# Optimization experiments

Measured on AMD Instinct MI355X. Metric: run time of the kernel, lower is better.

Reference implementation:

```python
import jax, jax.numpy as jnp
import numpy as np

N = 100000      # nodes
E = 1600000     # edges (avg degree 16)
IN_FEATS = 128
HEADS = 4
OUT_FEATS = 16
NEG_SLOPE = 0.2
EPS = 1e-16


def setup_inputs() -> dict:
    key = jax.random.key(0)
    k1, k2, k3, k4, k5, k6 = jax.random.split(key, 6)
    feat = jax.random.normal(k1, (N, IN_FEATS), dtype=jnp.float32)
    # xavier-ish scale for params
    W = jax.random.normal(k2, (IN_FEATS, HEADS * OUT_FEATS), dtype=jnp.float32) * 0.1
    attn_l = jax.random.normal(k3, (1, HEADS, OUT_FEATS), dtype=jnp.float32) * 0.1
    attn_r = jax.random.normal(k4, (1, HEADS, OUT_FEATS), dtype=jnp.float32) * 0.1
    src_index = jax.random.randint(k5, (E,), 0, N, dtype=jnp.int32)
    trg_index = jax.random.randint(k6, (E,), 0, N, dtype=jnp.int32)
    return {"feat": feat, "W": W, "attn_l": attn_l, "attn_r": attn_r,
            "src_index": src_index, "trg_index": trg_index}


def reference(feat, W, attn_l, attn_r, src_index, trg_index):
    # dropout layers are identity in eval mode
    n = feat.shape[0]
    h = (feat @ W).reshape(n, HEADS, OUT_FEATS)            # [N,H,F]
    el = jnp.sum(h * attn_l, axis=-1)                      # [N,H]
    er = jnp.sum(h * attn_r, axis=-1)                      # [N,H]
    s = el[src_index] + er[trg_index]                      # [E,H] edge scores
    s = jnp.where(s > 0, s, NEG_SLOPE * s)                 # LeakyReLU(0.2)
    # neighborhood-aware softmax over incoming edges of each target node
    s = s - jnp.max(s)                                     # global max shift (as in source)
    e = jnp.exp(s)                                         # [E,H]
    denom = jax.ops.segment_sum(e, trg_index, num_segments=n)  # [N,H]
    attn = e / (denom[trg_index] + EPS)                    # [E,H]
    # weighted aggregation of lifted source features into target nodes
    msg = h[src_index] * attn[:, :, None]                  # [E,H,F]
    h_prime = jax.ops.segment_sum(msg, trg_index, num_segments=n)  # [N,H,F]
    return h_prime.reshape(n, HEADS * OUT_FEATS)
```

## Files before the change

kernel.cpp:

```cpp
#include <hip/hip_runtime.h>

typedef unsigned short ushort_t;
typedef __attribute__((ext_vector_type(8))) short bf16x8;
typedef __attribute__((ext_vector_type(4))) float f32x4v;

static __device__ __forceinline__ float bf2f(ushort_t u) {
  union { unsigned int i; float f; } v; v.i = ((unsigned int)u) << 16; return v.f;
}
static __device__ __forceinline__ ushort_t f2bf(float f) {
  union { float f; unsigned int i; } v; v.f = f;
  unsigned int r = v.i + 0x7FFFu + ((v.i >> 16) & 1u);
  return (ushort_t)(r >> 16);
}
static __device__ __forceinline__ float leaky(float s) {
  return s > 0.f ? s : 0.2f * s;
}

__global__ __launch_bounds__(256) void packw_hist(
    const float* __restrict__ W, const float* __restrict__ attnl,
    const float* __restrict__ attnr, ushort_t* __restrict__ wfrag,
    const int* __restrict__ trg, int E, int nbkt,
    int* __restrict__ blockHist, int nb3, int epb)
{
  const int b = blockIdx.x;
  const int t = threadIdx.x;
  if (b == nb3) {
    const int kc = t >> 6, l = t & 63;
    const int q = l >> 4, n = l & 15;
    #pragma unroll
    for (int tile = 0; tile < 5; ++tile) {
      #pragma unroll
      for (int j = 0; j < 8; ++j) {
        const int k = kc * 32 + q * 8 + j;
        float v = 0.f;
        if (tile < 4) {
          v = W[k * 64 + tile * 16 + n];
        } else if (n < 4) {
          for (int f = 0; f < 16; ++f)
            v += W[k * 64 + n * 16 + f] * attnl[n * 16 + f];
        } else if (n < 8) {
          const int hd = n - 4;
          for (int f = 0; f < 16; ++f)
            v += W[k * 64 + hd * 16 + f] * attnr[hd * 16 + f];
        }
        wfrag[((tile * 4 + kc) * 64 + l) * 8 + j] = f2bf(v);
      }
    }
    return;
  }
  __shared__ int hist[256];
  hist[t] = 0;
  __syncthreads();
  const int start = b * epb;
  const int end = min(start + epb, E);
  for (int e = start + t; e < end; e += 256)
    atomicAdd(&hist[trg[e] >> 9], 1);
  __syncthreads();
  if (t < nbkt) blockHist[b * nbkt + t] = hist[t];
}

__global__ __launch_bounds__(64) void bucket_scan(
    int* __restrict__ blockHist, int nb3, int nbkt, int* __restrict__ colTotal)
{
  const int b = blockIdx.x;
  const int l = threadIdx.x;
  int carry = 0;
  for (int r = 0; r * 64 < nb3; ++r) {
    const int i = r * 64 + l;
    int v = (i < nb3) ? blockHist[i * nbkt + b] : 0;
    int incl = v;
    #pragma unroll
    for (int d = 1; d < 64; d <<= 1) {
      int u = __shfl_up(incl, d, 64);
      if (l >= d) incl += u;
    }
    if (i < nb3) blockHist[i * nbkt + b] = carry + incl - v;
    carry += __shfl(incl, 63, 64);
  }
  if (l == 0) colTotal[b] = carry;
}

__global__ __launch_bounds__(64) void bucket_base(
    const int* __restrict__ colTotal, int nbkt, int* __restrict__ bucketBase,
    int* __restrict__ rowoff, int N, int E)
{
  const int l = threadIdx.x;
  int carry = 0;
  for (int r = 0; r * 64 < nbkt; ++r) {
    const int i = r * 64 + l;
    int v = (i < nbkt) ? colTotal[i] : 0;
    int incl = v;
    #pragma unroll
    for (int d = 1; d < 64; d <<= 1) {
      int u = __shfl_up(incl, d, 64);
      if (l >= d) incl += u;
    }
    if (i < nbkt) bucketBase[i] = carry + incl - v;
    carry += __shfl(incl, 63, 64);
  }
  if (l == 0) { bucketBase[nbkt] = carry; rowoff[N] = E; }
}

__global__ __launch_bounds__(256) void bucket_scatter(
    const int* __restrict__ src, const int* __restrict__ trg, int E, int nbkt,
    const int* __restrict__ blockHist, const int* __restrict__ bucketBase,
    unsigned int* __restrict__ binned, int epb)
{
  __shared__ int cursor[256];
  const int t = threadIdx.x, b = blockIdx.x;
  if (t < nbkt) cursor[t] = bucketBase[t] + blockHist[b * nbkt + t];
  __syncthreads();
  const int start = b * epb;
  const int end = min(start + epb, E);
  for (int e = start + t; e < end; e += 256) {
    const int ti = trg[e];
    const int bkt = ti >> 9;
    const int pos = atomicAdd(&cursor[bkt], 1);
    binned[pos] = ((unsigned int)src[e] << 9) | (unsigned int)(ti & 511);
  }
}

__global__ __launch_bounds__(256) void gat_linear(
    const float* __restrict__ feat, const ushort_t* __restrict__ wfrag,
    ushort_t* __restrict__ h_out, float* __restrict__ el, float* __restrict__ er,
    float* __restrict__ blockmax2, int N)
{
  __shared__ ushort_t sFb[64 * 136];
  __shared__ float wmax[8];
  const int t = threadIdx.x;
  const int b = blockIdx.x;
  const int w = t >> 6, l = t & 63;
  const int q = l >> 4, m = l & 15;

  const float4* gF = (const float4*)(feat + (size_t)b * 64 * 128);
  #pragma unroll
  for (int i = 0; i < 8; ++i) {
    const int idx = i * 256 + t;
    const int node = idx >> 5, off = idx & 31;
    float4 v = make_float4(0.f, 0.f, 0.f, 0.f);
    if (b * 64 + node < N) v = gF[idx];
    unsigned int p0 = ((unsigned int)f2bf(v.y) << 16) | f2bf(v.x);
    unsigned int p1 = ((unsigned int)f2bf(v.w) << 16) | f2bf(v.z);
    *(uint2*)(sFb + node * 136 + off * 4) = make_uint2(p0, p1);
  }
  __syncthreads();

  bf16x8 a[4];
  const ushort_t* arow = sFb + (w * 16 + m) * 136 + q * 8;
  #pragma unroll
  for (int kc = 0; kc < 4; ++kc)
    a[kc] = *(const bf16x8*)(arow + kc * 32);

  #pragma unroll
  for (int tile = 0; tile < 4; ++tile) {
    f32x4v acc = {0.f, 0.f, 0.f, 0.f};
    #pragma unroll
    for (int kc = 0; kc < 4; ++kc) {
      bf16x8 bfr = *(const bf16x8*)(wfrag + ((tile * 4 + kc) * 64 + l) * 8);
      acc = __builtin_amdgcn_mfma_f32_16x16x32_bf16(a[kc], bfr, acc, 0, 0, 0);
    }
    #pragma unroll
    for (int r = 0; r < 4; ++r) {
      const int gn = b * 64 + w * 16 + q * 4 + r;
      if (gn < N) h_out[(size_t)gn * 64 + tile * 16 + m] = f2bf(acc[r]);
    }
  }

  f32x4v acc4 = {0.f, 0.f, 0.f, 0.f};
  #pragma unroll
  for (int kc = 0; kc < 4; ++kc) {
    bf16x8 bfr = *(const bf16x8*)(wfrag + ((4 * 4 + kc) * 64 + l) * 8);
    acc4 = __builtin_amdgcn_mfma_f32_16x16x32_bf16(a[kc], bfr, acc4, 0, 0, 0);
  }
  float mel = -1e30f, mer = -1e30f;
  #pragma unroll
  for (int r = 0; r < 4; ++r) {
    const int gn = b * 64 + w * 16 + q * 4 + r;
    const float v = acc4[r];
    if (m < 4) {
      if (gn < N) el[gn * 4 + m] = v;
      mel = fmaxf(mel, v);
    } else if (m < 8) {
      if (gn < N) er[gn * 4 + (m - 4)] = v;
      mer = fmaxf(mer, v);
    }
  }
  #pragma unroll
  for (int o = 1; o <= 32; o <<= 1) {
    mel = fmaxf(mel, __shfl_xor(mel, o, 64));
    mer = fmaxf(mer, __shfl_xor(mer, o, 64));
  }
  if (l == 0) { wmax[w * 2] = mel; wmax[w * 2 + 1] = mer; }
  __syncthreads();
  if (t == 0) {
    float aa = fmaxf(fmaxf(wmax[0], wmax[2]), fmaxf(wmax[4], wmax[6]));
    float cc = fmaxf(fmaxf(wmax[1], wmax[3]), fmaxf(wmax[5], wmax[7]));
    blockmax2[b * 2] = aa;
    blockmax2[b * 2 + 1] = cc;
  }
}

__global__ __launch_bounds__(512) void fine_scatter(
    const unsigned int* __restrict__ binned, const int* __restrict__ bucketBase,
    int* __restrict__ rowoff, int* __restrict__ csrsrc, int N,
    const float* __restrict__ blockmax2, int nbL, float* __restrict__ gmaxM)
{
  __shared__ int cnt[512];
  __shared__ int ws[8];
  __shared__ float wmg[16];
  const int t = threadIdx.x, b = blockIdx.x;
  const int l = t & 63, w = t >> 6;
  const int base = bucketBase[b];
  const int end = bucketBase[b + 1];
  cnt[t] = 0;
  if (b == 0) {
    float mel = -1e30f, mer = -1e30f;
    for (int i = t; i < nbL; i += 512) {
      mel = fmaxf(mel, blockmax2[i * 2]);
      mer = fmaxf(mer, blockmax2[i * 2 + 1]);
    }
    #pragma unroll
    for (int o = 1; o <= 32; o <<= 1) {
      mel = fmaxf(mel, __shfl_xor(mel, o, 64));
      mer = fmaxf(mer, __shfl_xor(mer, o, 64));
    }
    if (l == 0) { wmg[w * 2] = mel; wmg[w * 2 + 1] = mer; }
  }
  __syncthreads();
  if (b == 0 && t == 0) {
    float aa = -1e30f, cc = -1e30f;
    for (int i = 0; i < 8; ++i) {
      aa = fmaxf(aa, wmg[i * 2]);
      cc = fmaxf(cc, wmg[i * 2 + 1]);
    }
    gmaxM[0] = fmaxf(0.f, aa + cc);
  }
  for (int i = base + t; i < end; i += 512)
    atomicAdd(&cnt[binned[i] & 511u], 1);
  __syncthreads();
  const int v = cnt[t];
  int incl = v;
  #pragma unroll
  for (int d = 1; d < 64; d <<= 1) {
    int u = __shfl_up(incl, d, 64);
    if (l >= d) incl += u;
  }
  if (l == 63) ws[w] = incl;
  __syncthreads();
  int woff = 0;
  for (int i = 0; i < w; ++i) woff += ws[i];
  const int loc = woff + incl - v;
  cnt[t] = loc;
  const int gt = b * 512 + t;
  if (gt < N) rowoff[gt] = base + loc;
  __syncthreads();
  for (int i = base + t; i < end; i += 512) {
    const unsigned int pv = binned[i];
    const int lt = (int)(pv & 511u);
    const int pos = base + atomicAdd(&cnt[lt], 1);
    csrsrc[pos] = (int)(pv >> 9);
  }
}

#define FMA8(hv, p) do { \
  union { unsigned int i; float f; } c_; \
  c_.i = (hv).x << 16;          a0 += c_.f * (p); \
  c_.i = (hv).x & 0xffff0000u;  a1 += c_.f * (p); \
  c_.i = (hv).y << 16;          a2 += c_.f * (p); \
  c_.i = (hv).y & 0xffff0000u;  a3 += c_.f * (p); \
  c_.i = (hv).z << 16;          a4 += c_.f * (p); \
  c_.i = (hv).z & 0xffff0000u;  a5 += c_.f * (p); \
  c_.i = (hv).w << 16;          a6 += c_.f * (p); \
  c_.i = (hv).w & 0xffff0000u;  a7 += c_.f * (p); \
} while (0)

__global__ __launch_bounds__(256) void gat_agg(
    const int* __restrict__ csrsrc, const int* __restrict__ rowoff,
    const float4* __restrict__ el4, const float4* __restrict__ er4,
    const ushort_t* __restrict__ hbf, const float* __restrict__ gmaxM,
    float* __restrict__ out, int N)
{
  __shared__ float sP[4 * 64 * 4];
  __shared__ int sS[4 * 64];
  const int t = threadIdx.x;
  const int l = t & 63;
  const int w = t >> 6;
  const int n = blockIdx.x * 4 + w;
  if (n >= N) return;
  const int rg = l >> 3;
  const int cg = l & 7;
  const int hd2 = cg >> 1;
  const int start = rowoff[n];
  const int end = rowoff[n + 1];
  const float M = gmaxM[0];
  const float4 ern = er4[n];
  float* sPw = sP + w * 256;
  int* sSw = sS + w * 64;
  const ushort_t* hcg = hbf + cg * 8;

  float a0 = 0.f, a1 = 0.f, a2 = 0.f, a3 = 0.f;
  float a4 = 0.f, a5 = 0.f, a6 = 0.f, a7 = 0.f;
  float a8 = 0.f;

  for (int base = start; base < end; base += 64) {
    const int cnt = min(64, end - base);
    int sn = 0;
    float4 pv = make_float4(0.f, 0.f, 0.f, 0.f);
    if (l < cnt) {
      sn = csrsrc[base + l];
      const float4 a = el4[sn];
      pv.x = __expf(leaky(a.x + ern.x) - M);
      pv.y = __expf(leaky(a.y + ern.y) - M);
      pv.z = __expf(leaky(a.z + ern.z) - M);
      pv.w = __expf(leaky(a.w + ern.w) - M);
    }
    *(float4*)(sPw + l * 4) = pv;
    sSw[l] = sn;

    for (int j = 0; j < cnt; j += 16) {
      const int sA = sSw[j + rg];
      const int sB = sSw[j + 8 + rg];
      const float pA = sPw[(j + rg) * 4 + hd2];
      const float pB = sPw[(j + 8 + rg) * 4 + hd2];
      const uint4 hA = *(const uint4*)(hcg + (size_t)sA * 64);
      const uint4 hB = *(const uint4*)(hcg + (size_t)sB * 64);
      FMA8(hA, pA);
      FMA8(hB, pB);
      a8 += pA + pB;
    }
  }

  #pragma unroll
  for (int o = 8; o <= 32; o <<= 1) {
    a0 += __shfl_xor(a0, o, 64); a1 += __shfl_xor(a1, o, 64);
    a2 += __shfl_xor(a2, o, 64); a3 += __shfl_xor(a3, o, 64);
    a4 += __shfl_xor(a4, o, 64); a5 += __shfl_xor(a5, o, 64);
    a6 += __shfl_xor(a6, o, 64); a7 += __shfl_xor(a7, o, 64);
    a8 += __shfl_xor(a8, o, 64);
  }
  if (rg == 0) {
    const float r = 1.0f / (a8 + 1e-16f);
    float4* orow = (float4*)(out + (size_t)n * 64 + cg * 8);
    orow[0] = make_float4(a0 * r, a1 * r, a2 * r, a3 * r);
    orow[1] = make_float4(a4 * r, a5 * r, a6 * r, a7 * r);
  }
}

extern "C" void kernel_launch(void* const* d_in, const int* in_sizes, int n_in,
                              void* d_out, int out_size, void* d_ws, size_t ws_size,
                              hipStream_t stream) {
  const float* feat  = (const float*)d_in[0];
  const float* W     = (const float*)d_in[1];
  const float* attnl = (const float*)d_in[2];
  const float* attnr = (const float*)d_in[3];
  const int* src = (const int*)d_in[4];
  const int* trg = (const int*)d_in[5];
  float* out = (float*)d_out;

  const int N = in_sizes[0] / 128;
  const int E = in_sizes[4];

  const int nbL  = (N + 63) / 64;
  const int nbkt = (N + 511) >> 9;

  char* p = (char*)d_ws;
  auto take = [&](size_t bytes) -> char* {
    char* r = p;
    p += (bytes + 255) & ~(size_t)255;
    return r;
  };
  ushort_t* h_bf  = (ushort_t*)take((size_t)N * 64 * 2);
  float* el       = (float*)take((size_t)N * 16);
  float* er       = (float*)take((size_t)N * 16);
  int* rowoff     = (int*)take((size_t)(N + 1) * 4);
  int* csrsrc     = (int*)take((size_t)E * 4);
  unsigned int* binned = (unsigned int*)take((size_t)E * 4);
  ushort_t* wfrag = (ushort_t*)take(5 * 4 * 64 * 8 * 2);
  int* colTotal   = (int*)take((size_t)nbkt * 4);
  int* bucketBase = (int*)take((size_t)(nbkt + 1) * 4);
  float* blockmax2 = (float*)take((size_t)nbL * 2 * 4);
  float* gmaxM    = (float*)take(256);

  const size_t used = (size_t)(p - (char*)d_ws);
  const size_t avail = (ws_size > used + 512) ? (ws_size - used - 512) : 0;
  int nb3 = (int)(avail / ((size_t)nbkt * 4));
  if (nb3 > 800) nb3 = 800;
  if (nb3 < 64) nb3 = 64;
  int epb = (E + nb3 - 1) / nb3;
  nb3 = (E + epb - 1) / epb;
  int* blockHist  = (int*)take((size_t)nb3 * nbkt * 4);

  packw_hist<<<nb3 + 1, 256, 0, stream>>>(W, attnl, attnr, wfrag,
                                          trg, E, nbkt, blockHist, nb3, epb);
  bucket_scan<<<nbkt, 64, 0, stream>>>(blockHist, nb3, nbkt, colTotal);
  bucket_base<<<1, 64, 0, stream>>>(colTotal, nbkt, bucketBase, rowoff, N, E);
  bucket_scatter<<<nb3, 256, 0, stream>>>(src, trg, E, nbkt, blockHist,
                                          bucketBase, binned, epb);
  gat_linear<<<nbL, 256, 0, stream>>>(feat, wfrag, h_bf, el, er,
                                      blockmax2, N);
  fine_scatter<<<nbkt, 512, 0, stream>>>(binned, bucketBase, rowoff, csrsrc,
                                         N, blockmax2, nbL, gmaxM);
  gat_agg<<<(N + 3) / 4, 256, 0, stream>>>(csrsrc, rowoff, (const float4*)el,
                                           (const float4*)er, h_bf,
                                           gmaxM, out, N);
}
```

Before: 204.2 us.

## Process four target nodes per wavefront in GAT aggregation

The aggregation kernel now assigns four destination nodes to each 64-lane wavefront, with 16 lanes per node, instead of one node per wavefront. Edge scores for all four nodes are computed together in 16-edge chunks, and each lane accumulates two nodes' partial sums. The goal is to stop wasting lanes when the average degree is about 16, where a 64-edge chunk was mostly empty. The cost is that each wavefront loops to the largest degree among its four nodes, so skewed degrees cause idle work, and register use rises from holding two accumulator sets.

```diff
diff --git a/kernel.cpp b/kernel.cpp
--- a/kernel.cpp
+++ b/kernel.cpp
@@ -262,16 +262,16 @@
   }
 }
 
-#define FMA8(hv, p) do { \
+#define UNPACK_FMA(hv, p, acc) do { \
   union { unsigned int i; float f; } c_; \
-  c_.i = (hv).x << 16;          a0 += c_.f * (p); \
-  c_.i = (hv).x & 0xffff0000u;  a1 += c_.f * (p); \
-  c_.i = (hv).y << 16;          a2 += c_.f * (p); \
-  c_.i = (hv).y & 0xffff0000u;  a3 += c_.f * (p); \
-  c_.i = (hv).z << 16;          a4 += c_.f * (p); \
-  c_.i = (hv).z & 0xffff0000u;  a5 += c_.f * (p); \
-  c_.i = (hv).w << 16;          a6 += c_.f * (p); \
-  c_.i = (hv).w & 0xffff0000u;  a7 += c_.f * (p); \
+  c_.i = (hv).x << 16;          acc[0] += c_.f * (p); \
+  c_.i = (hv).x & 0xffff0000u;  acc[1] += c_.f * (p); \
+  c_.i = (hv).y << 16;          acc[2] += c_.f * (p); \
+  c_.i = (hv).y & 0xffff0000u;  acc[3] += c_.f * (p); \
+  c_.i = (hv).z << 16;          acc[4] += c_.f * (p); \
+  c_.i = (hv).z & 0xffff0000u;  acc[5] += c_.f * (p); \
+  c_.i = (hv).w << 16;          acc[6] += c_.f * (p); \
+  c_.i = (hv).w & 0xffff0000u;  acc[7] += c_.f * (p); \
 } while (0)
 
 __global__ __launch_bounds__(256) void gat_agg(
@@ -285,64 +285,89 @@
   const int t = threadIdx.x;
   const int l = t & 63;
   const int w = t >> 6;
-  const int n = blockIdx.x * 4 + w;
-  if (n >= N) return;
+  const int nbase = blockIdx.x * 16 + w * 4;
   const int rg = l >> 3;
   const int cg = l & 7;
   const int hd2 = cg >> 1;
-  const int start = rowoff[n];
-  const int end = rowoff[n + 1];
+  const int ks = l >> 4;
+  const int le = l & 15;
   const float M = gmaxM[0];
-  const float4 ern = er4[n];
   float* sPw = sP + w * 256;
   int* sSw = sS + w * 64;
   const ushort_t* hcg = hbf + cg * 8;
 
-  float a0 = 0.f, a1 = 0.f, a2 = 0.f, a3 = 0.f;
-  float a4 = 0.f, a5 = 0.f, a6 = 0.f, a7 = 0.f;
-  float a8 = 0.f;
-
-  for (int base = start; base < end; base += 64) {
-    const int cnt = min(64, end - base);
+  const int nk = nbase + ks;
+  const int rs = rowoff[min(nk, N)];
+  const int re = rowoff[min(nk + 1, N)];
+  const float4 ernk = (rs < re) ? er4[nk]
+                                : make_float4(0.f, 0.f, 0.f, 0.f);
+  int deg = re - rs;
+  deg = max(deg, __shfl_xor(deg, 16, 64));
+  deg = max(deg, __shfl_xor(deg, 32, 64));
+  const int chunks = (deg + 15) >> 4;
+
+  float aA[8] = {0.f,0.f,0.f,0.f,0.f,0.f,0.f,0.f};
+  float aB[8] = {0.f,0.f,0.f,0.f,0.f,0.f,0.f,0.f};
+  float dA = 0.f, dB = 0.f;
+
+  for (int c = 0; c < chunks; ++c) {
     int sn = 0;
     float4 pv = make_float4(0.f, 0.f, 0.f, 0.f);
-    if (l < cnt) {
-      sn = csrsrc[base + l];
+    const int ei = rs + c * 16 + le;
+    if (ei < re) {
+      sn = csrsrc[ei];
       const float4 a = el4[sn];
-      pv.x = __expf(leaky(a.x + ern.x) - M);
-      pv.y = __expf(leaky(a.y + ern.y) - M);
-      pv.z = __expf(leaky(a.z + ern.z) - M);
-      pv.w = __expf(leaky(a.w + ern.w) - M);
+      pv.x = __expf(leaky(a.x + ernk.x) - M);
+      pv.y = __expf(leaky(a.y + ernk.y) - M);
+      pv.z = __expf(leaky(a.z + ernk.z) - M);
+      pv.w = __expf(leaky(a.w + ernk.w) - M);
     }
     *(float4*)(sPw + l * 4) = pv;
     sSw[l] = sn;
 
-    for (int j = 0; j < cnt; j += 16) {
-      const int sA = sSw[j + rg];
-      const int sB = sSw[j + 8 + rg];
-      const float pA = sPw[(j + rg) * 4 + hd2];
-      const float pB = sPw[(j + 8 + rg) * 4 + hd2];
+    const int rem = min(deg - c * 16, 16);
+    const int jmax = (rem + 3) >> 2;
+    for (int j = 0; j < jmax; ++j) {
+      const int iA = ((rg >> 2) * 16) + (rg & 3) + j * 4;
+      const int iB = iA + 32;
+      const int sA = sSw[iA];
+      const int sB = sSw[iB];
+      const float pA = sPw[iA * 4 + hd2];
+      const float pB = sPw[iB * 4 + hd2];
       const uint4 hA = *(const uint4*)(hcg + (size_t)sA * 64);
       const uint4 hB = *(const uint4*)(hcg + (size_t)sB * 64);
-      FMA8(hA, pA);
-      FMA8(hB, pB);
-      a8 += pA + pB;
-    }
-  }
-
-  #pragma unroll
-  for (int o = 8; o <= 32; o <<= 1) {
-    a0 += __shfl_xor(a0, o, 64); a1 += __shfl_xor(a1, o, 64);
-    a2 += __shfl_xor(a2, o, 64); a3 += __shfl_xor(a3, o, 64);
-    a4 += __shfl_xor(a4, o, 64); a5 += __shfl_xor(a5, o, 64);
-    a6 += __shfl_xor(a6, o, 64); a7 += __shfl_xor(a7, o, 64);
-    a8 += __shfl_xor(a8, o, 64);
-  }
-  if (rg == 0) {
-    const float r = 1.0f / (a8 + 1e-16f);
-    float4* orow = (float4*)(out + (size_t)n * 64 + cg * 8);
-    orow[0] = make_float4(a0 * r, a1 * r, a2 * r, a3 * r);
-    orow[1] = make_float4(a4 * r, a5 * r, a6 * r, a7 * r);
+      UNPACK_FMA(hA, pA, aA);
+      UNPACK_FMA(hB, pB, aB);
+      dA += pA;
+      dB += pB;
+    }
+  }
+
+  #pragma unroll
+  for (int o = 8; o <= 16; o <<= 1) {
+    #pragma unroll
+    for (int i = 0; i < 8; ++i) {
+      aA[i] += __shfl_xor(aA[i], o, 64);
+      aB[i] += __shfl_xor(aB[i], o, 64);
+    }
+    dA += __shfl_xor(dA, o, 64);
+    dB += __shfl_xor(dB, o, 64);
+  }
+  if ((rg & 3) == 0) {
+    const int nA = nbase + (rg >> 2);
+    const int nB = nA + 2;
+    const float rA = 1.0f / (dA + 1e-16f);
+    const float rB = 1.0f / (dB + 1e-16f);
+    if (nA < N) {
+      float4* orow = (float4*)(out + (size_t)nA * 64 + cg * 8);
+      orow[0] = make_float4(aA[0] * rA, aA[1] * rA, aA[2] * rA, aA[3] * rA);
+      orow[1] = make_float4(aA[4] * rA, aA[5] * rA, aA[6] * rA, aA[7] * rA);
+    }
+    if (nB < N) {
+      float4* orow = (float4*)(out + (size_t)nB * 64 + cg * 8);
+      orow[0] = make_float4(aB[0] * rB, aB[1] * rB, aB[2] * rB, aB[3] * rB);
+      orow[1] = make_float4(aB[4] * rB, aB[5] * rB, aB[6] * rB, aB[7] * rB);
+    }
   }
 }
 
@@ -400,7 +425,7 @@
                                       blockmax2, N);
   fine_scatter<<<nbkt, 512, 0, stream>>>(binned, bucketBase, rowoff, csrsrc,
                                          N, blockmax2, nbL, gmaxM);
-  gat_agg<<<(N + 3) / 4, 256, 0, stream>>>(csrsrc, rowoff, (const float4*)el,
-                                           (const float4*)er, h_bf,
-                                           gmaxM, out, N);
-}
+  gat_agg<<<(N + 15) / 16, 256, 0, stream>>>(csrsrc, rowoff, (const float4*)el,
+                                             (const float4*)er, h_bf,
+                                             gmaxM, out, N);
+}
```

After: 202.5 us. No clear change (-0.8%).
